# Kernel tuning notes

Hardware: AMD Instinct MI355X
Metric: run time of the kernel (lower is better)

Reference implementation:

```python
import jax, jax.numpy as jnp
import numpy as np

B, T, I, H = 64, 2048, 128, 256

def setup_inputs() -> dict:
    key = jax.random.key(0)
    k1, k2, k3 = jax.random.split(key, 3)
    x = jax.random.normal(k1, (B, T, I), dtype=jnp.float32)
    # Linear(input_size+hidden_size -> hidden_size), Kaiming-uniform-ish scale
    bound = 1.0 / np.sqrt(I + H)
    W = jax.random.uniform(k2, (I + H, H), dtype=jnp.float32, minval=-bound, maxval=bound)
    b = jax.random.uniform(k3, (H,), dtype=jnp.float32, minval=-bound, maxval=bound)
    return {"x": x, "W": W, "b": b}

def reference(x, W, b):
    # Elman step: h' = sigmoid([x_t, h] @ W + b)
    Wx, Wh = W[:I], W[I:]  # split so we avoid the concat per step
    h0 = jnp.zeros((x.shape[0], Wh.shape[1]), dtype=x.dtype)
    xT = jnp.swapaxes(x, 0, 1)  # [T, B, I]
    # precompute x projections in one big GEMM; recurrence only does h @ Wh
    xproj = xT @ Wx + b  # [T, B, H]
    def step(h, xp):
        h_new = jax.nn.sigmoid(xp + h @ Wh)
        return h_new, h_new
    _, hs = jax.lax.scan(step, h0, xproj)
    return hs  # [T, B, H], matches torch.stack(hidden_states)
```

## Files before the change

### kernel.cpp

```cpp
#include <hip/hip_runtime.h>

#define T_LEN 2048
#define B_SZ  64
#define I_DIM 128
#define H_DIM 256

typedef _Float16 f16;
typedef _Float16 f16x8 __attribute__((ext_vector_type(8)));
typedef float    f32x4 __attribute__((ext_vector_type(4)));
typedef int      i32x4 __attribute__((ext_vector_type(4)));

__device__ __forceinline__ float fast_sigmoid(float z) {
  return __builtin_amdgcn_rcpf(1.0f + __expf(-z));
}

#define WG_BARRIER() do {                                  \
  asm volatile("s_waitcnt lgkmcnt(0)" ::: "memory");       \
  __builtin_amdgcn_s_barrier();                            \
  asm volatile("" ::: "memory");                           \
  __builtin_amdgcn_sched_barrier(0);                       \
} while (0)

__global__ __launch_bounds__(256) void xproj_kernel(
    const float* __restrict__ x, const float* __restrict__ W,
    const float* __restrict__ bias, float* __restrict__ out) {
  const int b    = blockIdx.y;
  const int tc   = blockIdx.x * 128;
  const int w    = threadIdx.x >> 6;
  const int lane = threadIdx.x & 63;
  const int cl   = lane & 15;
  const int kh   = lane >> 4;

  f16x8 Bf[4][4];
#pragma unroll
  for (int g = 0; g < 4; ++g) {
    const int c = 64 * w + 16 * g + cl;
#pragma unroll
    for (int q = 0; q < 4; ++q)
#pragma unroll
      for (int j = 0; j < 8; ++j)
        Bf[g][q][j] = (f16)W[(32 * q + 8 * kh + j) * H_DIM + c];
  }
  float bv[4];
#pragma unroll
  for (int g = 0; g < 4; ++g) bv[g] = bias[64 * w + 16 * g + cl];

#pragma unroll 1
  for (int tb = 0; tb < 128; tb += 16) {
    const int t0 = tc + tb;
    const float* xrow = x + ((size_t)b * T_LEN + (t0 + cl)) * I_DIM + 8 * kh;
    f16x8 Af[4];
#pragma unroll
    for (int q = 0; q < 4; ++q) {
      float4 u0 = *(const float4*)(xrow + 32 * q);
      float4 u1 = *(const float4*)(xrow + 32 * q + 4);
      f16x8 a;
      a[0] = (f16)u0.x; a[1] = (f16)u0.y; a[2] = (f16)u0.z; a[3] = (f16)u0.w;
      a[4] = (f16)u1.x; a[5] = (f16)u1.y; a[6] = (f16)u1.z; a[7] = (f16)u1.w;
      Af[q] = a;
    }
#pragma unroll
    for (int g = 0; g < 4; ++g) {
      f32x4 acc = {0.f, 0.f, 0.f, 0.f};
#pragma unroll
      for (int q = 0; q < 4; ++q)
        acc = __builtin_amdgcn_mfma_f32_16x16x32_f16(Af[q], Bf[g][q], acc, 0, 0, 0);
#pragma unroll
      for (int j = 0; j < 4; ++j) {
        const int t = t0 + 4 * kh + j;
        out[((size_t)t * B_SZ + b) * H_DIM + 64 * w + 16 * g + cl] = acc[j] + bv[g];
      }
    }
  }
}

#define MFMAI8(A, B, C) __builtin_amdgcn_mfma_i32_16x16x64_i8((A), (B), (C), 0, 0, 0)

#define RNN_STEP(tt, pp, RB) do {                                            \
  if ((cl & 3) == 0) {                                                       \
    _Pragma("unroll")                                                        \
    for (int q = 0; q < 4; ++q)                                              \
      Aq[q] = *(const i32x4*)&hbuf8[RB][64 * q + 16 * kh];                   \
  }                                                                          \
  i32x4 a0 = MFMAI8(Aq[0], Bq[0][0], Zacc);                                  \
  i32x4 a1 = MFMAI8(Aq[0], Bq[1][0], Zacc);                                  \
  i32x4 a2 = MFMAI8(Aq[0], Bq[2][0], Zacc);                                  \
  i32x4 a3 = MFMAI8(Aq[0], Bq[3][0], Zacc);                                  \
  _Pragma("unroll")                                                          \
  for (int q = 1; q < 4; ++q) {                                              \
    a0 = MFMAI8(Aq[q], Bq[0][q], a0);                                        \
    a1 = MFMAI8(Aq[q], Bq[1][q], a1);                                        \
    a2 = MFMAI8(Aq[q], Bq[2][q], a2);                                        \
    a3 = MFMAI8(Aq[q], Bq[3][q], a3);                                        \
  }                                                                          \
  int idot = g1 ? a1[0] : a0[0];                                             \
  idot = g2 ? a2[0] : idot;                                                  \
  idot = g3 ? a3[0] : idot;                                                  \
  float hh = fast_sigmoid(__builtin_fmaf((float)idot, INVS, zoff + (pp)));   \
  int hq = (int)__builtin_rintf(__builtin_fmaf(hh, 254.0f, -127.0f));        \
  hbuf8[(RB) ^ 1][colx] = (signed char)hq;                                   \
  WG_BARRIER();                                                              \
  op[(size_t)(tt) * rowstride] = hh;                                         \
} while (0)

#define SW_SCALE 2490.0f
#define INVS (1.0f / (254.0f * SW_SCALE))

__global__ __launch_bounds__(256, 1) void rnn_kernel(
    const float* __restrict__ W, float* out) {
  const int b    = blockIdx.x;
  const int tid  = threadIdx.x;
  const int w    = tid >> 6;
  const int lane = tid & 63;
  const int cl   = lane & 15;
  const int kh   = lane >> 4;

  __shared__ __align__(16) signed char hbuf8[2][H_DIM];
  hbuf8[0][tid] = (signed char)-127;
  hbuf8[1][tid] = (signed char)-127;

  i32x4 Bq[4][4];
#pragma unroll
  for (int g = 0; g < 4; ++g) {
    const int c = 64 * w + 16 * g + cl;
#pragma unroll
    for (int q = 0; q < 4; ++q) {
#pragma unroll
      for (int d = 0; d < 4; ++d) {
        int dw = 0;
#pragma unroll
        for (int j = 0; j < 4; ++j) {
          const int k = 64 * q + 16 * kh + 4 * d + j;
          const int qv = (int)__builtin_rintf(W[(I_DIM + k) * H_DIM + c] * SW_SCALE);
          dw |= (qv & 0xff) << (8 * j);
        }
        Bq[g][q][d] = dw;
      }
    }
  }

  int cs = 0;
#pragma unroll 4
  for (int k = 0; k < H_DIM; ++k)
    cs += (int)__builtin_rintf(W[(I_DIM + k) * H_DIM + tid] * SW_SCALE);
  const float zoff = 127.0f * (float)cs * INVS;

  i32x4 Aq[4];
#pragma unroll
  for (int q = 0; q < 4; ++q) Aq[q] = (i32x4){0, 0, 0, 0};

  const i32x4 Zacc = {0, 0, 0, 0};

  const bool g1 = (lane >> 4) == 1;
  const bool g2 = (lane >> 4) == 2;
  const bool g3 = (lane >> 4) == 3;

  const int    colx = tid;
  const size_t rowstride = (size_t)B_SZ * H_DIM;
  float* op = out + (size_t)b * H_DIM + colx;

  __syncthreads();

  float p0 = op[0 * rowstride];
  float p1 = op[1 * rowstride];
  float p2 = op[2 * rowstride];
  float p3 = op[3 * rowstride];

#pragma unroll 1
  for (int t = 0; t < T_LEN; t += 4) {
    float n0 = op[(size_t)((t + 4 < T_LEN) ? t + 4 : T_LEN - 1) * rowstride];
    RNN_STEP(t + 0, p0, 0); p0 = n0;
    float n1 = op[(size_t)((t + 5 < T_LEN) ? t + 5 : T_LEN - 1) * rowstride];
    RNN_STEP(t + 1, p1, 1); p1 = n1;
    float n2 = op[(size_t)((t + 6 < T_LEN) ? t + 6 : T_LEN - 1) * rowstride];
    RNN_STEP(t + 2, p2, 0); p2 = n2;
    float n3 = op[(size_t)((t + 7 < T_LEN) ? t + 7 : T_LEN - 1) * rowstride];
    RNN_STEP(t + 3, p3, 1); p3 = n3;
  }
}

extern "C" void kernel_launch(void* const* d_in, const int* in_sizes, int n_in,
                              void* d_out, int out_size, void* d_ws, size_t ws_size,
                              hipStream_t stream) {
  (void)in_sizes; (void)n_in; (void)d_ws; (void)ws_size; (void)out_size;
  const float* x    = (const float*)d_in[0];
  const float* W    = (const float*)d_in[1];
  const float* bias = (const float*)d_in[2];
  float* out = (float*)d_out;

  xproj_kernel<<<dim3(16, 64), 256, 0, stream>>>(x, W, bias, out);
  rnn_kernel<<<64, 256, 0, stream>>>(W, out);
}
```

Before: 666.9 us.

## Split RNN recurrence across 8 waves with two-column-group MFMA per wave

Raises the recurrence block from 4 to 8 waves, so each wave handles 32 hidden columns (two 16-column MFMA groups) and splits the K reduction into two independent accumulation chains summed at the end. This shortens the serial MFMA dependency chain per step and drops one of the per-lane selects. Only the first 32 lanes of each wave write hidden state and outputs, so half the lanes do redundant work and the barrier now covers twice as many waves. The loop also peels its last iteration to remove the clamped prefetch index and uses pointer increments for stores.

```diff
diff --git a/kernel.cpp b/kernel.cpp
--- a/kernel.cpp
+++ b/kernel.cpp
@@ -76,37 +76,37 @@
 
 #define MFMAI8(A, B, C) __builtin_amdgcn_mfma_i32_16x16x64_i8((A), (B), (C), 0, 0, 0)
 
-#define RNN_STEP(tt, pp, RB) do {                                            \
-  if ((cl & 3) == 0) {                                                       \
-    _Pragma("unroll")                                                        \
-    for (int q = 0; q < 4; ++q)                                              \
-      Aq[q] = *(const i32x4*)&hbuf8[RB][64 * q + 16 * kh];                   \
+#define SW_SCALE 2490.0f
+#define INVS (1.0f / (254.0f * SW_SCALE))
+#define RS (B_SZ * H_DIM)
+
+#define RNN_STEP(pp, RB) do {                                                \
+  if (rdlane) {                                                              \
+    Aq0 = *(const i32x4*)&hbuf8[RB][rd0];                                    \
+    Aq1 = *(const i32x4*)&hbuf8[RB][rd1];                                    \
+    Aq2 = *(const i32x4*)&hbuf8[RB][rd2];                                    \
+    Aq3 = *(const i32x4*)&hbuf8[RB][rd3];                                    \
   }                                                                          \
-  i32x4 a0 = MFMAI8(Aq[0], Bq[0][0], Zacc);                                  \
-  i32x4 a1 = MFMAI8(Aq[0], Bq[1][0], Zacc);                                  \
-  i32x4 a2 = MFMAI8(Aq[0], Bq[2][0], Zacc);                                  \
-  i32x4 a3 = MFMAI8(Aq[0], Bq[3][0], Zacc);                                  \
-  _Pragma("unroll")                                                          \
-  for (int q = 1; q < 4; ++q) {                                              \
-    a0 = MFMAI8(Aq[q], Bq[0][q], a0);                                        \
-    a1 = MFMAI8(Aq[q], Bq[1][q], a1);                                        \
-    a2 = MFMAI8(Aq[q], Bq[2][q], a2);                                        \
-    a3 = MFMAI8(Aq[q], Bq[3][q], a3);                                        \
-  }                                                                          \
-  int idot = g1 ? a1[0] : a0[0];                                             \
-  idot = g2 ? a2[0] : idot;                                                  \
-  idot = g3 ? a3[0] : idot;                                                  \
+  i32x4 a0L = MFMAI8(Aq0, Bq[0][0], Zacc);                                   \
+  i32x4 a1L = MFMAI8(Aq0, Bq[1][0], Zacc);                                   \
+  i32x4 a0H = MFMAI8(Aq2, Bq[0][2], Zacc);                                   \
+  i32x4 a1H = MFMAI8(Aq2, Bq[1][2], Zacc);                                   \
+  a0L = MFMAI8(Aq1, Bq[0][1], a0L);                                          \
+  a1L = MFMAI8(Aq1, Bq[1][1], a1L);                                          \
+  a0H = MFMAI8(Aq3, Bq[0][3], a0H);                                          \
+  a1H = MFMAI8(Aq3, Bq[1][3], a1H);                                          \
+  int i0 = a0L[0] + a0H[0];                                                  \
+  int i1 = a1L[0] + a1H[0];                                                  \
+  int idot = g1 ? i1 : i0;                                                   \
   float hh = fast_sigmoid(__builtin_fmaf((float)idot, INVS, zoff + (pp)));   \
   int hq = (int)__builtin_rintf(__builtin_fmaf(hh, 254.0f, -127.0f));        \
-  hbuf8[(RB) ^ 1][colx] = (signed char)hq;                                   \
+  if (act) hbuf8[(RB) ^ 1][colx] = (signed char)hq;                          \
   WG_BARRIER();                                                              \
-  op[(size_t)(tt) * rowstride] = hh;                                         \
+  if (act) *opSt = hh;                                                       \
+  opSt += RS;                                                                \
 } while (0)
 
-#define SW_SCALE 2490.0f
-#define INVS (1.0f / (254.0f * SW_SCALE))
-
-__global__ __launch_bounds__(256, 1) void rnn_kernel(
+__global__ __launch_bounds__(512, 2) void rnn_kernel(
     const float* __restrict__ W, float* out) {
   const int b    = blockIdx.x;
   const int tid  = threadIdx.x;
@@ -116,13 +116,19 @@
   const int kh   = lane >> 4;
 
   __shared__ __align__(16) signed char hbuf8[2][H_DIM];
-  hbuf8[0][tid] = (signed char)-127;
-  hbuf8[1][tid] = (signed char)-127;
-
-  i32x4 Bq[4][4];
-#pragma unroll
-  for (int g = 0; g < 4; ++g) {
-    const int c = 64 * w + 16 * g + cl;
+
+  const bool act  = (lane < 32);
+  const int  colx = 32 * w + (lane & 31);
+
+  if (act) {
+    hbuf8[0][colx] = (signed char)-127;
+    hbuf8[1][colx] = (signed char)-127;
+  }
+
+  i32x4 Bq[2][4];
+#pragma unroll
+  for (int g = 0; g < 2; ++g) {
+    const int c = 32 * w + 16 * g + cl;
 #pragma unroll
     for (int q = 0; q < 4; ++q) {
 #pragma unroll
@@ -142,22 +148,25 @@
   int cs = 0;
 #pragma unroll 4
   for (int k = 0; k < H_DIM; ++k)
-    cs += (int)__builtin_rintf(W[(I_DIM + k) * H_DIM + tid] * SW_SCALE);
+    cs += (int)__builtin_rintf(W[(I_DIM + k) * H_DIM + colx] * SW_SCALE);
   const float zoff = 127.0f * (float)cs * INVS;
 
-  i32x4 Aq[4];
-#pragma unroll
-  for (int q = 0; q < 4; ++q) Aq[q] = (i32x4){0, 0, 0, 0};
-
+  i32x4 Aq0 = {0, 0, 0, 0}, Aq1 = {0, 0, 0, 0};
+  i32x4 Aq2 = {0, 0, 0, 0}, Aq3 = {0, 0, 0, 0};
   const i32x4 Zacc = {0, 0, 0, 0};
 
-  const bool g1 = (lane >> 4) == 1;
-  const bool g2 = (lane >> 4) == 2;
-  const bool g3 = (lane >> 4) == 3;
-
-  const int    colx = tid;
-  const size_t rowstride = (size_t)B_SZ * H_DIM;
-  float* op = out + (size_t)b * H_DIM + colx;
+  const bool rdlane = ((cl & 11) == 0);
+  const int  rd0 = 0   + 16 * kh;
+  const int  rd1 = 64  + 16 * kh;
+  const int  rd2 = 128 + 16 * kh;
+  const int  rd3 = 192 + 16 * kh;
+
+  const bool g1 = ((lane >> 4) & 1) != 0;
+
+  const size_t rowstride = RS;
+  float* op   = out + (size_t)b * H_DIM + colx;
+  float* opSt = op;
+  const float* opPre = op + 4 * rowstride;
 
   __syncthreads();
 
@@ -167,16 +176,21 @@
   float p3 = op[3 * rowstride];
 
 #pragma unroll 1
-  for (int t = 0; t < T_LEN; t += 4) {
-    float n0 = op[(size_t)((t + 4 < T_LEN) ? t + 4 : T_LEN - 1) * rowstride];
-    RNN_STEP(t + 0, p0, 0); p0 = n0;
-    float n1 = op[(size_t)((t + 5 < T_LEN) ? t + 5 : T_LEN - 1) * rowstride];
-    RNN_STEP(t + 1, p1, 1); p1 = n1;
-    float n2 = op[(size_t)((t + 6 < T_LEN) ? t + 6 : T_LEN - 1) * rowstride];
-    RNN_STEP(t + 2, p2, 0); p2 = n2;
-    float n3 = op[(size_t)((t + 7 < T_LEN) ? t + 7 : T_LEN - 1) * rowstride];
-    RNN_STEP(t + 3, p3, 1); p3 = n3;
-  }
+  for (int it = 0; it < (T_LEN - 4) / 4; ++it) {
+    float n0 = opPre[0 * rowstride];
+    RNN_STEP(p0, 0); p0 = n0;
+    float n1 = opPre[1 * rowstride];
+    RNN_STEP(p1, 1); p1 = n1;
+    float n2 = opPre[2 * rowstride];
+    RNN_STEP(p2, 0); p2 = n2;
+    float n3 = opPre[3 * rowstride];
+    RNN_STEP(p3, 1); p3 = n3;
+    opPre += 4 * rowstride;
+  }
+  RNN_STEP(p0, 0);
+  RNN_STEP(p1, 1);
+  RNN_STEP(p2, 0);
+  RNN_STEP(p3, 1);
 }
 
 extern "C" void kernel_launch(void* const* d_in, const int* in_sizes, int n_in,
@@ -189,5 +203,5 @@
   float* out = (float*)d_out;
 
   xproj_kernel<<<dim3(16, 64), 256, 0, stream>>>(x, W, bias, out);
-  rnn_kernel<<<64, 256, 0, stream>>>(W, out);
-}
+  rnn_kernel<<<64, 512, 0, stream>>>(W, out);
+}
```

Result: slower. 692.9 us (+3.9%).
